# Optimization experiments

Hardware: AMD Instinct MI355X
Metric: run time of the kernel (lower is better)

The kernel has to match this reference:

```python
import jax, jax.numpy as jnp
import numpy as np

NEG_INF = -1e30  # stand-in for float('-inf'); avoids inf-inf NaN edge cases, same softmax result


def setup_inputs() -> dict:
    key = jax.random.key(0)
    k1, k2, k3, k4, k5 = jax.random.split(key, 5)
    B, T, C, H = 16, 2048, 200, 64
    x = jax.random.normal(k1, (B, T, C), dtype=jnp.float32)
    # padding mask over key positions, broadcastable to [B, T, T]
    padding_mask = jax.random.randint(k2, (B, 1, T), 0, 2, dtype=jnp.int32)
    # nn.Linear(n_embd, head_size, bias=False) weights, stored as [C, H] so y = x @ W
    Wk = jax.random.normal(k3, (C, H), dtype=jnp.float32) * (C ** -0.5)
    Wq = jax.random.normal(k4, (C, H), dtype=jnp.float32) * (C ** -0.5)
    Wv = jax.random.normal(k5, (C, H), dtype=jnp.float32) * (C ** -0.5)
    return {"x": x, "padding_mask": padding_mask, "Wk": Wk, "Wq": Wq, "Wv": Wv}


def reference(x, padding_mask, Wk, Wq, Wv):
    # x: [B,T,C]; padding_mask: [B,1,T] (0 = padded key position)
    k = x @ Wk  # [B,T,H]
    q = x @ Wq  # [B,T,H]
    v = x @ Wv  # [B,T,H]
    scale = k.shape[-1] ** -0.5
    wei = jnp.einsum("bqh,bkh->bqk", q, k) * scale  # [B,T,T]
    # mask padded key columns before softmax
    wei = jnp.where(padding_mask == 0, NEG_INF, wei)
    wei = jax.nn.softmax(wei, axis=-1)
    # mask padded query rows (transpose of padding mask) to exact zero after softmax
    mask_t = jnp.swapaxes(padding_mask, -2, -1)  # [B,T,1]
    wei = jnp.where(mask_t == 0, 0.0, wei)
    # dropout is identity in eval mode
    out = jnp.einsum("bqk,bkh->bqh", wei, v)  # [B,T,H]
    return out
```

## Files before the change

kernel.cpp:

```cpp
#include <hip/hip_runtime.h>


typedef __attribute__((ext_vector_type(8))) __bf16 bf16x8;
typedef __attribute__((ext_vector_type(4))) __bf16 bf16x4;
typedef __attribute__((ext_vector_type(4))) float f32x4;

#define T_SEQ 2048
#define C_DIM 200
#define H_DIM 64
#define BT_TOT 32768
#define QKV_ELEMS 2097152
#define PPAD 72
#define OPAD 68
#define WTF_FULL 36864
#define WTF_ELEMS 38400
#define WTF_A_ELEMS 24576
#define LOG2E 1.44269504088896f

__global__ void prep_w(const float* __restrict__ Wk, const float* __restrict__ Wq,
                       const float* __restrict__ Wv, __bf16* __restrict__ WtF) {
    int idx = blockIdx.x * 256 + threadIdx.x;
    if (idx >= WTF_ELEMS) return;
    int w, c, h;
    if (idx < WTF_FULL) {
        int j = idx & 7, lane = (idx >> 3) & 63;
        int chunk = idx >> 9;
        int t = chunk & 3, rest = chunk >> 2;
        w = rest % 3; int ks = rest / 3;
        c = ks * 32 + (lane >> 4) * 8 + j;
        h = t * 16 + (lane & 15);
    } else {
        int i2 = idx - WTF_FULL;
        int j = i2 & 7, l15 = (i2 >> 3) & 15, t = (i2 >> 7) & 3;
        w = i2 >> 9;
        c = 192 + j;
        h = t * 16 + l15;
    }
    const float* W = (w == 0) ? Wq : (w == 1) ? Wk : Wv;
    float val = W[c * H_DIM + h];
    if (w == 0) val *= 0.125f * LOG2E;
    WtF[idx] = (__bf16)val;
}

__global__ __launch_bounds__(128) void qkv_proj(const float* __restrict__ x,
                                                const __bf16* __restrict__ WtF,
                                                __bf16* __restrict__ qb,
                                                __bf16* __restrict__ kb,
                                                __bf16* __restrict__ vT) {
    __shared__ __bf16 Wl[WTF_A_ELEMS];

    const int tid = threadIdx.x;
    const int wave = tid >> 6, lane = tid & 63, l15 = lane & 15, quad = lane >> 4;
    const int m0b = blockIdx.x * 64;
    const int row0 = m0b + wave * 32;

    f32x4 acc[3][2][4] = {};

    #pragma unroll
    for (int i = 0; i < 24; ++i) {
        const int c = i * 128 + tid;
        *(bf16x8*)(Wl + c * 8) = *(const bf16x8*)(WtF + c * 8);
    }
    __syncthreads();
    #pragma unroll
    for (int ks = 0; ks < 4; ++ks) {
        bf16x8 a[2];
        #pragma unroll
        for (int mt = 0; mt < 2; ++mt) {
            const float* xr = x + (size_t)(row0 + mt * 16 + l15) * C_DIM + ks * 32 + quad * 8;
            const float4 f0 = *(const float4*)xr;
            const float4 f1 = *(const float4*)(xr + 4);
            a[mt][0]=(__bf16)f0.x; a[mt][1]=(__bf16)f0.y; a[mt][2]=(__bf16)f0.z; a[mt][3]=(__bf16)f0.w;
            a[mt][4]=(__bf16)f1.x; a[mt][5]=(__bf16)f1.y; a[mt][6]=(__bf16)f1.z; a[mt][7]=(__bf16)f1.w;
        }
        #pragma unroll
        for (int w = 0; w < 3; ++w)
            #pragma unroll
            for (int t = 0; t < 4; ++t) {
                const bf16x8 bf = *(const bf16x8*)(Wl + ((ks * 12 + w * 4 + t) << 9) + lane * 8);
                acc[w][0][t] = __builtin_amdgcn_mfma_f32_16x16x32_bf16(a[0], bf, acc[w][0][t], 0, 0, 0);
                acc[w][1][t] = __builtin_amdgcn_mfma_f32_16x16x32_bf16(a[1], bf, acc[w][1][t], 0, 0, 0);
            }
    }
    __syncthreads();

    #pragma unroll
    for (int i = 0; i < 14; ++i) {
        const int c = i * 128 + tid;
        if (c < 1728)
            *(bf16x8*)(Wl + c * 8) = *(const bf16x8*)(WtF + WTF_A_ELEMS + c * 8);
    }
    __syncthreads();
    #pragma unroll
    for (int ks = 4; ks < 7; ++ks) {
        bf16x8 a[2];
        #pragma unroll
        for (int mt = 0; mt < 2; ++mt) {
            if (ks < 6 || quad == 0) {
                const float* xr = x + (size_t)(row0 + mt * 16 + l15) * C_DIM + ks * 32 + quad * 8;
                const float4 f0 = *(const float4*)xr;
                const float4 f1 = *(const float4*)(xr + 4);
                a[mt][0]=(__bf16)f0.x; a[mt][1]=(__bf16)f0.y; a[mt][2]=(__bf16)f0.z; a[mt][3]=(__bf16)f0.w;
                a[mt][4]=(__bf16)f1.x; a[mt][5]=(__bf16)f1.y; a[mt][6]=(__bf16)f1.z; a[mt][7]=(__bf16)f1.w;
            } else {
                #pragma unroll
                for (int j = 0; j < 8; ++j) a[mt][j] = (__bf16)0.f;
            }
        }
        #pragma unroll
        for (int w = 0; w < 3; ++w)
            #pragma unroll
            for (int t = 0; t < 4; ++t) {
                const int off = (ks < 6) ? (((ks - 4) * 12 + w * 4 + t) << 9) + lane * 8
                                         : 12288 + ((w * 4 + t) << 7) + l15 * 8;
                const bf16x8 bf = *(const bf16x8*)(Wl + off);
                acc[w][0][t] = __builtin_amdgcn_mfma_f32_16x16x32_bf16(a[0], bf, acc[w][0][t], 0, 0, 0);
                acc[w][1][t] = __builtin_amdgcn_mfma_f32_16x16x32_bf16(a[1], bf, acc[w][1][t], 0, 0, 0);
            }
    }

    #pragma unroll
    for (int mt = 0; mt < 2; ++mt)
        #pragma unroll
        for (int t = 0; t < 4; ++t)
            #pragma unroll
            for (int r = 0; r < 4; ++r) {
                const size_t m = row0 + mt * 16 + quad * 4 + r;
                qb[m * H_DIM + t * 16 + l15] = (__bf16)acc[0][mt][t][r];
                kb[m * H_DIM + t * 16 + l15] = (__bf16)acc[1][mt][t][r];
            }
    __syncthreads();
    #pragma unroll
    for (int mt = 0; mt < 2; ++mt)
        #pragma unroll
        for (int t = 0; t < 4; ++t)
            #pragma unroll
            for (int r = 0; r < 4; ++r)
                Wl[(t * 16 + l15) * 72 + wave * 32 + mt * 16 + quad * 4 + r] = (__bf16)acc[2][mt][t][r];
    __syncthreads();
    const int bb = m0b >> 11, tloc = m0b & 2047;
    #pragma unroll
    for (int i = 0; i < 4; ++i) {
        const int seg = i * 128 + tid;
        const int h = seg >> 3, s8 = seg & 7;
        *(bf16x8*)(vT + ((size_t)bb * H_DIM + h) * T_SEQ + tloc + s8 * 8) =
            *(const bf16x8*)(Wl + h * 72 + s8 * 8);
    }
}

__global__ __launch_bounds__(256, 2) void attn(const __bf16* __restrict__ qb,
                                               const __bf16* __restrict__ kb,
                                               const __bf16* __restrict__ vT,
                                               const int* __restrict__ pm,
                                               float* __restrict__ out) {
    __shared__ __align__(16) char arena[8192 + 36864];
    float* biasS = (float*)arena;

    const int tid = threadIdx.x;
    const int wave = tid >> 6, lane = tid & 63, l15 = lane & 15, quad = lane >> 4;
    const int ks = wave;
    const int b = blockIdx.y;
    const int q0 = blockIdx.x * 64;
    const size_t bT = (size_t)b * T_SEQ;

    for (int i = tid; i < 512; i += 256) {
        const int4 p4 = *(const int4*)(pm + bT + i * 4);
        biasS[i * 4 + 0] = p4.x ? 0.f : -1e30f;
        biasS[i * 4 + 1] = p4.y ? 0.f : -1e30f;
        biasS[i * 4 + 2] = p4.z ? 0.f : -1e30f;
        biasS[i * 4 + 3] = p4.w ? 0.f : -1e30f;
    }
    __syncthreads();

    bf16x8 qa[4][2];
    #pragma unroll
    for (int mt = 0; mt < 4; ++mt)
        #pragma unroll
        for (int s = 0; s < 2; ++s)
            qa[mt][s] = *(const bf16x8*)(qb + (bT + q0 + mt * 16 + l15) * H_DIM + s * 32 + quad * 8);

    __bf16* P = (__bf16*)(arena + 8192) + wave * (64 * PPAD);

    f32x4 oacc[4][4] = {};
    float lsum[4] = {0.f, 0.f, 0.f, 0.f};

    for (int kt = 0; kt < 8; ++kt) {
        const int key0 = ks * 512 + kt * 64;

        #pragma unroll
        for (int n = 0; n < 4; ++n) {
            const f32x4 bias = *(const f32x4*)(biasS + key0 + n * 16 + quad * 4);
            f32x4 s_[4];
            #pragma unroll
            for (int mt = 0; mt < 4; ++mt) s_[mt] = bias;
            #pragma unroll
            for (int s = 0; s < 2; ++s) {
                const bf16x8 kf = *(const bf16x8*)(kb + (bT + key0 + n * 16 + l15) * H_DIM + s * 32 + quad * 8);
                #pragma unroll
                for (int mt = 0; mt < 4; ++mt)
                    s_[mt] = __builtin_amdgcn_mfma_f32_16x16x32_bf16(kf, qa[mt][s], s_[mt], 0, 0, 0);
            }
            #pragma unroll
            for (int mt = 0; mt < 4; ++mt) {
                bf16x4 p4;
                #pragma unroll
                for (int r = 0; r < 4; ++r) {
                    const float e = exp2f(s_[mt][r]);
                    lsum[mt] += e;
                    p4[r] = (__bf16)e;
                }
                *(bf16x4*)(P + (mt * 16 + l15) * PPAD + n * 16 + quad * 4) = p4;
            }
        }

        bf16x8 pa[4][2];
        #pragma unroll
        for (int mt = 0; mt < 4; ++mt)
            #pragma unroll
            for (int s = 0; s < 2; ++s)
                pa[mt][s] = *(const bf16x8*)(P + (mt * 16 + l15) * PPAD + s * 32 + quad * 8);

        #pragma unroll
        for (int t = 0; t < 4; ++t) {
            #pragma unroll
            for (int s = 0; s < 2; ++s) {
                const bf16x8 vf = *(const bf16x8*)(vT + ((size_t)b * H_DIM + t * 16 + l15) * T_SEQ + key0 + s * 32 + quad * 8);
                #pragma unroll
                for (int mt = 0; mt < 4; ++mt)
                    oacc[mt][t] = __builtin_amdgcn_mfma_f32_16x16x32_bf16(pa[mt][s], vf, oacc[mt][t], 0, 0, 0);
            }
        }
    }

    #pragma unroll
    for (int mt = 0; mt < 4; ++mt) {
        lsum[mt] += __shfl_xor(lsum[mt], 16, 64);
        lsum[mt] += __shfl_xor(lsum[mt], 32, 64);
    }

    float* Ocomb = (float*)(arena + 8192);
    float* Lcomb = Ocomb + 64 * OPAD;

    __syncthreads();
    if (ks == 1) {
        #pragma unroll
        for (int mt = 0; mt < 4; ++mt) {
            #pragma unroll
            for (int t = 0; t < 4; ++t)
                #pragma unroll
                for (int r = 0; r < 4; ++r)
                    Ocomb[(mt * 16 + quad * 4 + r) * OPAD + t * 16 + l15] = oacc[mt][t][r];
            if (quad == 0) Lcomb[mt * 16 + l15] = lsum[mt];
        }
    }
    __syncthreads();
    if (ks == 2) {
        #pragma unroll
        for (int mt = 0; mt < 4; ++mt) {
            #pragma unroll
            for (int t = 0; t < 4; ++t)
                #pragma unroll
                for (int r = 0; r < 4; ++r)
                    Ocomb[(mt * 16 + quad * 4 + r) * OPAD + t * 16 + l15] += oacc[mt][t][r];
            if (quad == 0) Lcomb[mt * 16 + l15] += lsum[mt];
        }
    }
    __syncthreads();
    if (ks == 3) {
        #pragma unroll
        for (int mt = 0; mt < 4; ++mt) {
            #pragma unroll
            for (int t = 0; t < 4; ++t)
                #pragma unroll
                for (int r = 0; r < 4; ++r)
                    Ocomb[(mt * 16 + quad * 4 + r) * OPAD + t * 16 + l15] += oacc[mt][t][r];
            if (quad == 0) Lcomb[mt * 16 + l15] += lsum[mt];
        }
    }
    __syncthreads();
    if (ks == 0) {
        #pragma unroll
        for (int mt = 0; mt < 4; ++mt) {
            lsum[mt] += Lcomb[mt * 16 + l15];
            #pragma unroll
            for (int t = 0; t < 4; ++t)
                #pragma unroll
                for (int r = 0; r < 4; ++r)
                    oacc[mt][t][r] += Ocomb[(mt * 16 + quad * 4 + r) * OPAD + t * 16 + l15];
            #pragma unroll
            for (int r = 0; r < 4; ++r) {
                const int qpos = q0 + mt * 16 + quad * 4 + r;
                const float lv = __shfl(lsum[mt], quad * 4 + r, 64);
                const bool qvalid = biasS[qpos] == 0.f;
                const float inv = (qvalid && lv > 0.f) ? 1.f / lv : 0.f;
                #pragma unroll
                for (int t = 0; t < 4; ++t)
                    out[(bT + qpos) * H_DIM + t * 16 + l15] = oacc[mt][t][r] * inv;
            }
        }
    }
}

extern "C" void kernel_launch(void* const* d_in, const int* in_sizes, int n_in,
                              void* d_out, int out_size, void* d_ws, size_t ws_size,
                              hipStream_t stream) {
    const float* x  = (const float*)d_in[0];
    const int* pm   = (const int*)d_in[1];
    const float* Wk = (const float*)d_in[2];
    const float* Wq = (const float*)d_in[3];
    const float* Wv = (const float*)d_in[4];
    float* out = (float*)d_out;

    __bf16* qb  = (__bf16*)d_ws;
    __bf16* kb  = qb + QKV_ELEMS;
    __bf16* vT  = kb + QKV_ELEMS;
    __bf16* WtF = vT + QKV_ELEMS;

    prep_w<<<dim3((WTF_ELEMS + 255) / 256), dim3(256), 0, stream>>>(Wk, Wq, Wv, WtF);
    qkv_proj<<<dim3(BT_TOT / 64), dim3(128), 0, stream>>>(x, WtF, qb, kb, vT);
    attn<<<dim3(T_SEQ / 64, 16), dim3(256), 0, stream>>>(qb, kb, vT, pm, out);
}
```

Before: 126.1 us.

## Use four waves per QKV projection block and prefetch K/V fragments in attention

The QKV projection kernel now runs 256 threads per block, with each wave handling 16 rows instead of 32. This halves per-wave accumulator registers and spreads the shared-memory weight staging across more threads. In the attention kernel, K fragments for the next key tile are loaded into registers during the current iteration, and V fragments are loaded at the top of each iteration, so global-load latency overlaps with MFMA work. The cost is extra live vector registers in attention, which could hurt occupancy under the 2-blocks-per-SM launch bound.

```diff
diff --git a/kernel.cpp b/kernel.cpp
--- a/kernel.cpp
+++ b/kernel.cpp
@@ -42,7 +42,7 @@
     WtF[idx] = (__bf16)val;
 }
 
-__global__ __launch_bounds__(128) void qkv_proj(const float* __restrict__ x,
+__global__ __launch_bounds__(256) void qkv_proj(const float* __restrict__ x,
                                                 const __bf16* __restrict__ WtF,
                                                 __bf16* __restrict__ qb,
                                                 __bf16* __restrict__ kb,
@@ -52,60 +52,53 @@
     const int tid = threadIdx.x;
     const int wave = tid >> 6, lane = tid & 63, l15 = lane & 15, quad = lane >> 4;
     const int m0b = blockIdx.x * 64;
-    const int row0 = m0b + wave * 32;
-
-    f32x4 acc[3][2][4] = {};
-
-    #pragma unroll
-    for (int i = 0; i < 24; ++i) {
-        const int c = i * 128 + tid;
+    const int row0 = m0b + wave * 16;
+
+    f32x4 acc[3][4] = {};
+
+    #pragma unroll
+    for (int i = 0; i < 12; ++i) {
+        const int c = i * 256 + tid;
         *(bf16x8*)(Wl + c * 8) = *(const bf16x8*)(WtF + c * 8);
     }
     __syncthreads();
     #pragma unroll
     for (int ks = 0; ks < 4; ++ks) {
-        bf16x8 a[2];
-        #pragma unroll
-        for (int mt = 0; mt < 2; ++mt) {
-            const float* xr = x + (size_t)(row0 + mt * 16 + l15) * C_DIM + ks * 32 + quad * 8;
+        const float* xr = x + (size_t)(row0 + l15) * C_DIM + ks * 32 + quad * 8;
+        const float4 f0 = *(const float4*)xr;
+        const float4 f1 = *(const float4*)(xr + 4);
+        bf16x8 a;
+        a[0]=(__bf16)f0.x; a[1]=(__bf16)f0.y; a[2]=(__bf16)f0.z; a[3]=(__bf16)f0.w;
+        a[4]=(__bf16)f1.x; a[5]=(__bf16)f1.y; a[6]=(__bf16)f1.z; a[7]=(__bf16)f1.w;
+        #pragma unroll
+        for (int w = 0; w < 3; ++w)
+            #pragma unroll
+            for (int t = 0; t < 4; ++t) {
+                const bf16x8 bf = *(const bf16x8*)(Wl + ((ks * 12 + w * 4 + t) << 9) + lane * 8);
+                acc[w][t] = __builtin_amdgcn_mfma_f32_16x16x32_bf16(a, bf, acc[w][t], 0, 0, 0);
+            }
+    }
+    __syncthreads();
+
+    #pragma unroll
+    for (int i = 0; i < 7; ++i) {
+        const int c = i * 256 + tid;
+        if (c < 1728)
+            *(bf16x8*)(Wl + c * 8) = *(const bf16x8*)(WtF + WTF_A_ELEMS + c * 8);
+    }
+    __syncthreads();
+    #pragma unroll
+    for (int ks = 4; ks < 7; ++ks) {
+        bf16x8 a;
+        if (ks < 6 || quad == 0) {
+            const float* xr = x + (size_t)(row0 + l15) * C_DIM + ks * 32 + quad * 8;
             const float4 f0 = *(const float4*)xr;
             const float4 f1 = *(const float4*)(xr + 4);
-            a[mt][0]=(__bf16)f0.x; a[mt][1]=(__bf16)f0.y; a[mt][2]=(__bf16)f0.z; a[mt][3]=(__bf16)f0.w;
-            a[mt][4]=(__bf16)f1.x; a[mt][5]=(__bf16)f1.y; a[mt][6]=(__bf16)f1.z; a[mt][7]=(__bf16)f1.w;
-        }
-        #pragma unroll
-        for (int w = 0; w < 3; ++w)
-            #pragma unroll
-            for (int t = 0; t < 4; ++t) {
-                const bf16x8 bf = *(const bf16x8*)(Wl + ((ks * 12 + w * 4 + t) << 9) + lane * 8);
-                acc[w][0][t] = __builtin_amdgcn_mfma_f32_16x16x32_bf16(a[0], bf, acc[w][0][t], 0, 0, 0);
-                acc[w][1][t] = __builtin_amdgcn_mfma_f32_16x16x32_bf16(a[1], bf, acc[w][1][t], 0, 0, 0);
-            }
-    }
-    __syncthreads();
-
-    #pragma unroll
-    for (int i = 0; i < 14; ++i) {
-        const int c = i * 128 + tid;
-        if (c < 1728)
-            *(bf16x8*)(Wl + c * 8) = *(const bf16x8*)(WtF + WTF_A_ELEMS + c * 8);
-    }
-    __syncthreads();
-    #pragma unroll
-    for (int ks = 4; ks < 7; ++ks) {
-        bf16x8 a[2];
-        #pragma unroll
-        for (int mt = 0; mt < 2; ++mt) {
-            if (ks < 6 || quad == 0) {
-                const float* xr = x + (size_t)(row0 + mt * 16 + l15) * C_DIM + ks * 32 + quad * 8;
-                const float4 f0 = *(const float4*)xr;
-                const float4 f1 = *(const float4*)(xr + 4);
-                a[mt][0]=(__bf16)f0.x; a[mt][1]=(__bf16)f0.y; a[mt][2]=(__bf16)f0.z; a[mt][3]=(__bf16)f0.w;
-                a[mt][4]=(__bf16)f1.x; a[mt][5]=(__bf16)f1.y; a[mt][6]=(__bf16)f1.z; a[mt][7]=(__bf16)f1.w;
-            } else {
-                #pragma unroll
-                for (int j = 0; j < 8; ++j) a[mt][j] = (__bf16)0.f;
-            }
+            a[0]=(__bf16)f0.x; a[1]=(__bf16)f0.y; a[2]=(__bf16)f0.z; a[3]=(__bf16)f0.w;
+            a[4]=(__bf16)f1.x; a[5]=(__bf16)f1.y; a[6]=(__bf16)f1.z; a[7]=(__bf16)f1.w;
+        } else {
+            #pragma unroll
+            for (int j = 0; j < 8; ++j) a[j] = (__bf16)0.f;
         }
         #pragma unroll
         for (int w = 0; w < 3; ++w)
@@ -114,34 +107,29 @@
                 const int off = (ks < 6) ? (((ks - 4) * 12 + w * 4 + t) << 9) + lane * 8
                                          : 12288 + ((w * 4 + t) << 7) + l15 * 8;
                 const bf16x8 bf = *(const bf16x8*)(Wl + off);
-                acc[w][0][t] = __builtin_amdgcn_mfma_f32_16x16x32_bf16(a[0], bf, acc[w][0][t], 0, 0, 0);
-                acc[w][1][t] = __builtin_amdgcn_mfma_f32_16x16x32_bf16(a[1], bf, acc[w][1][t], 0, 0, 0);
+                acc[w][t] = __builtin_amdgcn_mfma_f32_16x16x32_bf16(a, bf, acc[w][t], 0, 0, 0);
             }
     }
 
     #pragma unroll
-    for (int mt = 0; mt < 2; ++mt)
-        #pragma unroll
-        for (int t = 0; t < 4; ++t)
-            #pragma unroll
-            for (int r = 0; r < 4; ++r) {
-                const size_t m = row0 + mt * 16 + quad * 4 + r;
-                qb[m * H_DIM + t * 16 + l15] = (__bf16)acc[0][mt][t][r];
-                kb[m * H_DIM + t * 16 + l15] = (__bf16)acc[1][mt][t][r];
-            }
-    __syncthreads();
-    #pragma unroll
-    for (int mt = 0; mt < 2; ++mt)
-        #pragma unroll
-        for (int t = 0; t < 4; ++t)
-            #pragma unroll
-            for (int r = 0; r < 4; ++r)
-                Wl[(t * 16 + l15) * 72 + wave * 32 + mt * 16 + quad * 4 + r] = (__bf16)acc[2][mt][t][r];
+    for (int t = 0; t < 4; ++t)
+        #pragma unroll
+        for (int r = 0; r < 4; ++r) {
+            const size_t m = row0 + quad * 4 + r;
+            qb[m * H_DIM + t * 16 + l15] = (__bf16)acc[0][t][r];
+            kb[m * H_DIM + t * 16 + l15] = (__bf16)acc[1][t][r];
+        }
+    __syncthreads();
+    #pragma unroll
+    for (int t = 0; t < 4; ++t)
+        #pragma unroll
+        for (int r = 0; r < 4; ++r)
+            Wl[(t * 16 + l15) * 72 + wave * 16 + quad * 4 + r] = (__bf16)acc[2][t][r];
     __syncthreads();
     const int bb = m0b >> 11, tloc = m0b & 2047;
     #pragma unroll
-    for (int i = 0; i < 4; ++i) {
-        const int seg = i * 128 + tid;
+    for (int i = 0; i < 2; ++i) {
+        const int seg = i * 256 + tid;
         const int h = seg >> 3, s8 = seg & 7;
         *(bf16x8*)(vT + ((size_t)bb * H_DIM + h) * T_SEQ + tloc + s8 * 8) =
             *(const bf16x8*)(Wl + h * 72 + s8 * 8);
@@ -180,12 +168,28 @@
             qa[mt][s] = *(const bf16x8*)(qb + (bT + q0 + mt * 16 + l15) * H_DIM + s * 32 + quad * 8);
 
     __bf16* P = (__bf16*)(arena + 8192) + wave * (64 * PPAD);
+    const __bf16* kbase = kb + bT * H_DIM;
+    const __bf16* vbase = vT + (size_t)b * H_DIM * T_SEQ;
 
     f32x4 oacc[4][4] = {};
     float lsum[4] = {0.f, 0.f, 0.f, 0.f};
 
+    bf16x8 kf[8];
+    #pragma unroll
+    for (int n = 0; n < 4; ++n)
+        #pragma unroll
+        for (int s = 0; s < 2; ++s)
+            kf[n * 2 + s] = *(const bf16x8*)(kbase + (ks * 512 + n * 16 + l15) * H_DIM + s * 32 + quad * 8);
+
     for (int kt = 0; kt < 8; ++kt) {
         const int key0 = ks * 512 + kt * 64;
+
+        bf16x8 vf[8];
+        #pragma unroll
+        for (int t = 0; t < 4; ++t)
+            #pragma unroll
+            for (int s = 0; s < 2; ++s)
+                vf[t * 2 + s] = *(const bf16x8*)(vbase + (size_t)(t * 16 + l15) * T_SEQ + key0 + s * 32 + quad * 8);
 
         #pragma unroll
         for (int n = 0; n < 4; ++n) {
@@ -194,12 +198,10 @@
             #pragma unroll
             for (int mt = 0; mt < 4; ++mt) s_[mt] = bias;
             #pragma unroll
-            for (int s = 0; s < 2; ++s) {
-                const bf16x8 kf = *(const bf16x8*)(kb + (bT + key0 + n * 16 + l15) * H_DIM + s * 32 + quad * 8);
+            for (int s = 0; s < 2; ++s)
                 #pragma unroll
                 for (int mt = 0; mt < 4; ++mt)
-                    s_[mt] = __builtin_amdgcn_mfma_f32_16x16x32_bf16(kf, qa[mt][s], s_[mt], 0, 0, 0);
-            }
+                    s_[mt] = __builtin_amdgcn_mfma_f32_16x16x32_bf16(kf[n * 2 + s], qa[mt][s], s_[mt], 0, 0, 0);
             #pragma unroll
             for (int mt = 0; mt < 4; ++mt) {
                 bf16x4 p4;
@@ -213,6 +215,13 @@
             }
         }
 
+        const int keyn = ks * 512 + ((kt < 7) ? kt + 1 : 7) * 64;
+        #pragma unroll
+        for (int n = 0; n < 4; ++n)
+            #pragma unroll
+            for (int s = 0; s < 2; ++s)
+                kf[n * 2 + s] = *(const bf16x8*)(kbase + (keyn + n * 16 + l15) * H_DIM + s * 32 + quad * 8);
+
         bf16x8 pa[4][2];
         #pragma unroll
         for (int mt = 0; mt < 4; ++mt)
@@ -221,15 +230,12 @@
                 pa[mt][s] = *(const bf16x8*)(P + (mt * 16 + l15) * PPAD + s * 32 + quad * 8);
 
         #pragma unroll
-        for (int t = 0; t < 4; ++t) {
-            #pragma unroll
-            for (int s = 0; s < 2; ++s) {
-                const bf16x8 vf = *(const bf16x8*)(vT + ((size_t)b * H_DIM + t * 16 + l15) * T_SEQ + key0 + s * 32 + quad * 8);
+        for (int t = 0; t < 4; ++t)
+            #pragma unroll
+            for (int s = 0; s < 2; ++s)
                 #pragma unroll
                 for (int mt = 0; mt < 4; ++mt)
-                    oacc[mt][t] = __builtin_amdgcn_mfma_f32_16x16x32_bf16(pa[mt][s], vf, oacc[mt][t], 0, 0, 0);
-            }
-        }
+                    oacc[mt][t] = __builtin_amdgcn_mfma_f32_16x16x32_bf16(pa[mt][s], vf[t * 2 + s], oacc[mt][t], 0, 0, 0);
     }
 
     #pragma unroll
@@ -317,6 +323,6 @@
     __bf16* WtF = vT + QKV_ELEMS;
 
     prep_w<<<dim3((WTF_ELEMS + 255) / 256), dim3(256), 0, stream>>>(Wk, Wq, Wv, WtF);
-    qkv_proj<<<dim3(BT_TOT / 64), dim3(128), 0, stream>>>(x, WtF, qb, kb, vT);
+    qkv_proj<<<dim3(BT_TOT / 64), dim3(256), 0, stream>>>(x, WtF, qb, kb, vT);
     attn<<<dim3(T_SEQ / 64, 16), dim3(256), 0, stream>>>(qb, kb, vT, pm, out);
 }
```

New measurement: 124.5 us. Within noise of the previous version (-1.3%).
